# Optimization experiments

Hardware: AMD Instinct MI355X
Metric: run time of the kernel (lower is better)

## Reference

```python
import jax, jax.numpy as jnp
import numpy as np


def _init_t_xy(end_x, end_y):
    t = jnp.arange(end_x * end_y, dtype=jnp.float32)
    return t % end_x, jnp.floor(t / end_x)


def _cis_cos_sin(freqs, t_x, t_y):
    # freqs: [2, H, D/4]; returns cos/sin of angles [H, N, D/2]
    fx = jnp.einsum('n,hd->hnd', t_x, freqs[0])
    fy = jnp.einsum('n,hd->hnd', t_y, freqs[1])
    ang = jnp.concatenate([fx, fy], axis=-1)
    return jnp.cos(ang), jnp.sin(ang)


def _rotate(x, c, s):
    # x: [B,H,N,D]; c,s: [H,N,D/2]; complex multiply in real arithmetic
    B, H, N, D = x.shape
    xr = x.reshape(B, H, N, D // 2, 2)
    x0, x1 = xr[..., 0], xr[..., 1]
    o0 = x0 * c[None] - x1 * s[None]
    o1 = x0 * s[None] + x1 * c[None]
    return jnp.stack([o0, o1], axis=-1).reshape(B, H, N, D)


def setup_inputs() -> dict:
    key = jax.random.key(0)
    k1, k2, k3, k4 = jax.random.split(key, 4)
    B, H, N, D = 2, 12, 2048, 64
    return {
        'q': jax.random.normal(k1, (B, H, N, D), dtype=jnp.float32),
        'b': jax.random.normal(k2, (B, H, N, D), dtype=jnp.float32),
        'rope_freqs': jax.random.normal(k3, (2, H, D // 4), dtype=jnp.float32),
        'weight': jax.random.uniform(k4, (1, H, 1, 1), dtype=jnp.float32),
        'end_x_xq': 64, 'end_y_xq': 32, 'end_x_xb': 64, 'end_y_xb': 32,
    }


def reference(q, b, rope_freqs, weight, end_x_xq, end_y_xq, end_x_xb, end_y_xb):
    t_x_xb, t_y_xb = _init_t_xy(end_x_xb, end_y_xb)
    t_x_xq, t_y_xq = _init_t_xy(end_x_xq, end_y_xq)
    # resample key-grid coordinates onto query grid
    t_x_xb = jnp.floor((t_x_xb + 0.5) / end_x_xb * end_x_xq - 0.5)
    t_y_xb = jnp.floor((t_y_xb + 0.5) / end_y_xb * end_y_xq - 0.5)
    ck, sk = _cis_cos_sin(rope_freqs, t_x_xb, t_y_xb)
    cq, sq = _cis_cos_sin(rope_freqs, t_x_xq, t_y_xq)
    # O(Nq*Nb) distance-decay mask, per-head decay rate
    dist = jnp.sqrt((t_x_xb[None, :] - t_x_xq[:, None]) ** 2
                    + (t_y_xb[None, :] - t_y_xq[:, None]) ** 2)
    delta = jnp.exp(-dist[None, None] * jax.nn.leaky_relu(weight))
    xq = _rotate(q, cq, sq)
    xb = _rotate(b, ck, sk)
    return jnp.einsum('bhnd,bhmd->bhnm', xq, xb) * delta
```

## Files before the change

kernel.cpp:

```cpp
#include <hip/hip_runtime.h>
#include <hip/hip_bf16.h>

#define BQ   2
#define NH   12
#define SEQ  2048
#define DIM  64
#define EXQ  64

#define TENSOR_ELEMS ((size_t)BQ * NH * SEQ * DIM)
#define ROPE_BLOCKS  6144

typedef __attribute__((ext_vector_type(8))) short short8;
typedef __attribute__((ext_vector_type(4))) float f32x4;

static __device__ __forceinline__ unsigned int pk2bf(float lo, float hi) {
    union { float f; unsigned int u; } a, b; a.f = lo; b.f = hi;
    unsigned int rl = (a.u + 0x7fffu + ((a.u >> 16) & 1u)) >> 16;
    unsigned int rh = (b.u + 0x7fffu + ((b.u >> 16) & 1u)) >> 16;
    return (rh << 16) | (rl & 0xffffu);
}

__global__ __launch_bounds__(256)
void rope_kernel(const float* __restrict__ qin,
                 const float* __restrict__ bin,
                 const float* __restrict__ freqs,
                 unsigned int* __restrict__ ws_u32)
{
    int t  = blockIdx.x * 256 + threadIdx.x;
    int p4 = t & 15;
    int n  = (t >> 4) & (SEQ - 1);
    int rest = t >> 15;
    int h    = rest % NH;
    int tb   = rest / NH;
    int tensor = tb >> 1;
    int b      = tb & 1;

    float tx = (float)(n & (EXQ - 1));
    float ty = (float)(n >> 6);

    int pr0 = 2 * p4;
    float f0, f1;
    if (p4 < 8) {
        f0 = freqs[h * 16 + pr0] * tx;
        f1 = freqs[h * 16 + pr0 + 1] * tx;
    } else {
        f0 = freqs[NH * 16 + h * 16 + (pr0 - 16)] * ty;
        f1 = freqs[NH * 16 + h * 16 + (pr0 - 15)] * ty;
    }

    const float* src = tensor ? bin : qin;
    size_t off = ((size_t)(b * NH + h) * SEQ + n) * DIM + 4 * p4;
    float4 v = *reinterpret_cast<const float4*>(src + off);

    float s0 = sinf(f0), c0 = cosf(f0);
    float s1 = sinf(f1), c1 = cosf(f1);

    float o0 = v.x * c0 - v.y * s0;
    float o1 = v.x * s0 + v.y * c0;
    float o2 = v.z * c1 - v.w * s1;
    float o3 = v.z * s1 + v.w * c1;

    uint2 packed;
    packed.x = pk2bf(o0, o1);
    packed.y = pk2bf(o2, o3);
    size_t uidx = (size_t)tensor * (TENSOR_ELEMS / 2) + (off >> 1);
    *reinterpret_cast<uint2*>(ws_u32 + uidx) = packed;
}

__global__ __launch_bounds__(256, 3)
void gemm_delta_kernel(const unsigned short* __restrict__ ws,
                       const float* __restrict__ weight,
                       float* __restrict__ out)
{
    __shared__ float lds[64 * 128];
    __shared__ float ltab[4 * 3 * 128];

    const int bh   = blockIdx.z;
    const int h    = bh % NH;
    const int lane = threadIdx.x & 63;
    const int wave = threadIdx.x >> 6;
    const int wr   = wave >> 1, wc = wave & 1;
    const int brow0 = blockIdx.y * 128;
    const int bcol0 = blockIdx.x * 128;
    const int row0 = brow0 + wr * 64;
    const int col0 = bcol0 + wc * 64;

    const unsigned short* xq = ws;
    const unsigned short* xb = ws + TENSOR_ELEMS;

    const int r16 = lane & 15;
    const int kg  = lane >> 4;

    const size_t base = (size_t)bh * SEQ * DIM;

    const float w  = weight[h];
    const float lw = w > 0.f ? w : 0.01f * w;
    const float scale = -lw * 1.44269504088896f;
    const int dymid = (bcol0 >> 6) - (brow0 >> 6);
    for (int e = threadIdx.x; e < 4 * 3 * 128; e += 256) {
        int x    = e & 127;
        int rest = e >> 7;
        int s    = rest / 3;
        int dyr  = rest - 3 * s;
        float dx = (float)(x + s - 63);
        float dy = (float)(dymid + dyr - 1);
        ltab[e] = exp2f(scale * sqrtf(dx * dx + dy * dy));
    }
    __syncthreads();

    f32x4 acc[4][4];
#pragma unroll
    for (int i = 0; i < 4; ++i)
#pragma unroll
        for (int j = 0; j < 4; ++j)
            acc[i][j] = (f32x4){0.f, 0.f, 0.f, 0.f};

#pragma unroll
    for (int kk = 0; kk < 2; ++kk) {
        short8 afr[4], bfr[4];
        int k = kk * 32 + kg * 8;
#pragma unroll
        for (int i = 0; i < 4; ++i) {
            int arw = row0 + i * 16 + r16;
            int bcl = col0 + i * 16 + r16;
            afr[i] = *reinterpret_cast<const short8*>(xq + base + (size_t)arw * DIM + k);
            bfr[i] = *reinterpret_cast<const short8*>(xb + base + (size_t)bcl * DIM + k);
        }
#pragma unroll
        for (int i = 0; i < 4; ++i)
#pragma unroll
            for (int j = 0; j < 4; ++j)
                acc[i][j] = __builtin_amdgcn_mfma_f32_16x16x32_bf16(
                    bfr[j], afr[i], acc[i][j], 0, 0, 0);
    }

    const int dyrel = (wc - wr) + 1;

#pragma unroll
    for (int half = 0; half < 2; ++half) {
        if (half) __syncthreads();
#pragma unroll
        for (int ii = 0; ii < 2; ++ii) {
            const int i  = half * 2 + ii;
            const int qx = i * 16 + r16;
            const int lrow = wr * 32 + ii * 16 + r16;
#pragma unroll
            for (int j = 0; j < 4; ++j) {
                int dxi_s = 63 - qx + kg * 4 + j * 16;
                int s     = dxi_s & 3;
                int tbase = dxi_s - s;
                f32x4 t = *reinterpret_cast<const f32x4*>(
                    &ltab[(s * 3 + dyrel) * 128 + tbase]);
                int col16 = wc * 16 + j * 4 + kg;
                int slot  = col16 ^ (lrow & 7);
                *reinterpret_cast<f32x4*>(&lds[lrow * 128 + slot * 4]) =
                    acc[i][j] * t;
            }
        }
        __syncthreads();
        const int c32 = lane & 31;
#pragma unroll
        for (int tI = 0; tI < 8; ++tI) {
            int lr = wave * 16 + tI * 2 + (lane >> 5);
            int slot = c32 ^ (lr & 7);
            f32x4 v = *reinterpret_cast<const f32x4*>(&lds[lr * 128 + slot * 4]);
            int wr_ = lr >> 5;
            int i   = half * 2 + ((lr >> 4) & 1);
            int grow = brow0 + wr_ * 64 + i * 16 + (lr & 15);
            float* op = out + ((size_t)bh * SEQ + grow) * SEQ + bcol0 + c32 * 4;
            __builtin_nontemporal_store(v, reinterpret_cast<f32x4*>(op));
        }
    }
}

extern "C" void kernel_launch(void* const* d_in, const int* in_sizes, int n_in,
                              void* d_out, int out_size, void* d_ws, size_t ws_size,
                              hipStream_t stream) {
    const float* q  = (const float*)d_in[0];
    const float* b  = (const float*)d_in[1];
    const float* fr = (const float*)d_in[2];
    const float* wt = (const float*)d_in[3];
    float* out = (float*)d_out;

    const size_t need_tensors = 2 * TENSOR_ELEMS * sizeof(unsigned short);
    if (ws_size < need_tensors) return;

    unsigned short* ws16 = (unsigned short*)d_ws;

    rope_kernel<<<ROPE_BLOCKS, 256, 0, stream>>>(q, b, fr, (unsigned int*)d_ws);

    dim3 grid(SEQ / 128, SEQ / 128, BQ * NH);
    gemm_delta_kernel<<<grid, 256, 0, stream>>>(ws16, wt, out);
}
```

Measured before the change: 104.5 us.

## Make GEMM-delta kernel persistent with prefetched fragments and register-computed decay

Replaces the 3D grid with 512 persistent blocks that each process 12 consecutive output tiles. The next tile's A/B fragments are prefetched during the epilogue, and the A panel is reused when the row panel is unchanged. The LDS decay table is dropped: decay factors are computed in registers per tile (28 exp2/sqrt per lane), and the whole 128x128 tile is staged through a doubled LDS buffer in one pass. The kernel is output-write bound, so the gain depends on overlapping stores with compute. Occupancy drops to 2 blocks per CU and register pressure rises.

After: 100.1 us. 1.04x faster.

```diff
diff --git a/kernel.cpp b/kernel.cpp
--- a/kernel.cpp
+++ b/kernel.cpp
@@ -9,6 +9,8 @@
 
 #define TENSOR_ELEMS ((size_t)BQ * NH * SEQ * DIM)
 #define ROPE_BLOCKS  6144
+#define PERS_BLOCKS  512
+#define TILES_PER_BLOCK 12
 
 typedef __attribute__((ext_vector_type(8))) short short8;
 typedef __attribute__((ext_vector_type(4))) float f32x4;
@@ -18,6 +20,11 @@
     unsigned int rl = (a.u + 0x7fffu + ((a.u >> 16) & 1u)) >> 16;
     unsigned int rh = (b.u + 0x7fffu + ((b.u >> 16) & 1u)) >> 16;
     return (rh << 16) | (rl & 0xffffu);
+}
+
+static __device__ __forceinline__ void wg_barrier_lds() {
+    asm volatile("s_waitcnt lgkmcnt(0)" ::: "memory");
+    __builtin_amdgcn_s_barrier();
 }
 
 __global__ __launch_bounds__(256)
@@ -67,107 +74,124 @@
     *reinterpret_cast<uint2*>(ws_u32 + uidx) = packed;
 }
 
-__global__ __launch_bounds__(256, 3)
+__global__ __launch_bounds__(256, 2)
 void gemm_delta_kernel(const unsigned short* __restrict__ ws,
                        const float* __restrict__ weight,
                        float* __restrict__ out)
 {
-    __shared__ float lds[64 * 128];
-    __shared__ float ltab[4 * 3 * 128];
-
-    const int bh   = blockIdx.z;
-    const int h    = bh % NH;
+    __shared__ float lds[128 * 128];
+
     const int lane = threadIdx.x & 63;
     const int wave = threadIdx.x >> 6;
     const int wr   = wave >> 1, wc = wave & 1;
-    const int brow0 = blockIdx.y * 128;
-    const int bcol0 = blockIdx.x * 128;
-    const int row0 = brow0 + wr * 64;
-    const int col0 = bcol0 + wc * 64;
+    const int r16  = lane & 15;
+    const int kg   = lane >> 4;
+    const int c32  = lane & 31;
 
     const unsigned short* xq = ws;
     const unsigned short* xb = ws + TENSOR_ELEMS;
 
-    const int r16 = lane & 15;
-    const int kg  = lane >> 4;
-
-    const size_t base = (size_t)bh * SEQ * DIM;
-
-    const float w  = weight[h];
-    const float lw = w > 0.f ? w : 0.01f * w;
-    const float scale = -lw * 1.44269504088896f;
-    const int dymid = (bcol0 >> 6) - (brow0 >> 6);
-    for (int e = threadIdx.x; e < 4 * 3 * 128; e += 256) {
-        int x    = e & 127;
-        int rest = e >> 7;
-        int s    = rest / 3;
-        int dyr  = rest - 3 * s;
-        float dx = (float)(x + s - 63);
-        float dy = (float)(dymid + dyr - 1);
-        ltab[e] = exp2f(scale * sqrtf(dx * dx + dy * dy));
-    }
-    __syncthreads();
-
-    f32x4 acc[4][4];
-#pragma unroll
-    for (int i = 0; i < 4; ++i)
-#pragma unroll
-        for (int j = 0; j < 4; ++j)
-            acc[i][j] = (f32x4){0.f, 0.f, 0.f, 0.f};
-
-#pragma unroll
-    for (int kk = 0; kk < 2; ++kk) {
-        short8 afr[4], bfr[4];
-        int k = kk * 32 + kg * 8;
+    short8 afr[2][4], bfr[2][4];
+    int last_panel = -1;
+
+    auto load_frags = [&](int g) {
+        int bh = g >> 8, rem = g & 255;
+        int trow = rem >> 4, tcol = rem & 15;
+        const size_t base = (size_t)bh * SEQ * DIM;
+        int panel = (bh << 4) | trow;
+        if (panel != last_panel) {
+            last_panel = panel;
+            int row0 = trow * 128 + wr * 64;
+#pragma unroll
+            for (int kk = 0; kk < 2; ++kk)
+#pragma unroll
+                for (int i = 0; i < 4; ++i) {
+                    int arw = row0 + i * 16 + r16;
+                    afr[kk][i] = *reinterpret_cast<const short8*>(
+                        xq + base + (size_t)arw * DIM + kk * 32 + kg * 8);
+                }
+        }
+        int col0 = tcol * 128 + wc * 64;
+#pragma unroll
+        for (int kk = 0; kk < 2; ++kk)
+#pragma unroll
+            for (int i = 0; i < 4; ++i) {
+                int bcl = col0 + i * 16 + r16;
+                bfr[kk][i] = *reinterpret_cast<const short8*>(
+                    xb + base + (size_t)bcl * DIM + kk * 32 + kg * 8);
+            }
+    };
+
+    int g0 = blockIdx.x * TILES_PER_BLOCK;
+    load_frags(g0);
+
+    for (int t = 0; t < TILES_PER_BLOCK; ++t) {
+        const int g    = g0 + t;
+        const int bh   = g >> 8, rem = g & 255;
+        const int trow = rem >> 4, tcol = rem & 15;
+        const int h    = bh % NH;
+        const int brow0 = trow * 128, bcol0 = tcol * 128;
+
+        f32x4 acc[4][4];
+#pragma unroll
+        for (int i = 0; i < 4; ++i)
+#pragma unroll
+            for (int j = 0; j < 4; ++j)
+                acc[i][j] = (f32x4){0.f, 0.f, 0.f, 0.f};
+#pragma unroll
+        for (int kk = 0; kk < 2; ++kk)
+#pragma unroll
+            for (int i = 0; i < 4; ++i)
+#pragma unroll
+                for (int j = 0; j < 4; ++j)
+                    acc[i][j] = __builtin_amdgcn_mfma_f32_16x16x32_bf16(
+                        bfr[kk][j], afr[kk][i], acc[i][j], 0, 0, 0);
+
+        {
+            float w  = weight[h];
+            float lw = w > 0.f ? w : 0.01f * w;
+            float scale = -lw * 1.44269504088896f;
+            float fdy = (float)(2 * (tcol - trow) + (wc - wr));
+            float dy2 = fdy * fdy;
+            f32x4 T[7];
+#pragma unroll
+            for (int d = 0; d < 7; ++d) {
+                float dx0 = (float)((d - 3) * 16 + kg * 4 - r16);
+#pragma unroll
+                for (int w_ = 0; w_ < 4; ++w_) {
+                    float dx = dx0 + (float)w_;
+                    T[d][w_] = exp2f(scale * sqrtf(dx * dx + dy2));
+                }
+            }
+#pragma unroll
+            for (int i = 0; i < 4; ++i)
+#pragma unroll
+                for (int j = 0; j < 4; ++j)
+                    acc[i][j] *= T[j - i + 3];
+        }
+
+        if (t + 1 < TILES_PER_BLOCK) load_frags(g + 1);
+        __builtin_amdgcn_sched_barrier(0);
+
+        wg_barrier_lds();
 #pragma unroll
         for (int i = 0; i < 4; ++i) {
-            int arw = row0 + i * 16 + r16;
-            int bcl = col0 + i * 16 + r16;
-            afr[i] = *reinterpret_cast<const short8*>(xq + base + (size_t)arw * DIM + k);
-            bfr[i] = *reinterpret_cast<const short8*>(xb + base + (size_t)bcl * DIM + k);
-        }
-#pragma unroll
-        for (int i = 0; i < 4; ++i)
-#pragma unroll
-            for (int j = 0; j < 4; ++j)
-                acc[i][j] = __builtin_amdgcn_mfma_f32_16x16x32_bf16(
-                    bfr[j], afr[i], acc[i][j], 0, 0, 0);
-    }
-
-    const int dyrel = (wc - wr) + 1;
-
-#pragma unroll
-    for (int half = 0; half < 2; ++half) {
-        if (half) __syncthreads();
-#pragma unroll
-        for (int ii = 0; ii < 2; ++ii) {
-            const int i  = half * 2 + ii;
-            const int qx = i * 16 + r16;
-            const int lrow = wr * 32 + ii * 16 + r16;
+            int lrow = wr * 64 + i * 16 + r16;
 #pragma unroll
             for (int j = 0; j < 4; ++j) {
-                int dxi_s = 63 - qx + kg * 4 + j * 16;
-                int s     = dxi_s & 3;
-                int tbase = dxi_s - s;
-                f32x4 t = *reinterpret_cast<const f32x4*>(
-                    &ltab[(s * 3 + dyrel) * 128 + tbase]);
-                int col16 = wc * 16 + j * 4 + kg;
-                int slot  = col16 ^ (lrow & 7);
-                *reinterpret_cast<f32x4*>(&lds[lrow * 128 + slot * 4]) =
-                    acc[i][j] * t;
+                int slot = (wc * 16 + j * 4 + kg) ^ (lrow & 7);
+                *reinterpret_cast<f32x4*>(&lds[lrow * 128 + slot * 4]) = acc[i][j];
             }
         }
-        __syncthreads();
-        const int c32 = lane & 31;
-#pragma unroll
-        for (int tI = 0; tI < 8; ++tI) {
-            int lr = wave * 16 + tI * 2 + (lane >> 5);
+        wg_barrier_lds();
+
+        const size_t obase = (size_t)bh * SEQ * SEQ;
+#pragma unroll
+        for (int tI = 0; tI < 16; ++tI) {
+            int lr = wave * 32 + tI * 2 + (lane >> 5);
             int slot = c32 ^ (lr & 7);
             f32x4 v = *reinterpret_cast<const f32x4*>(&lds[lr * 128 + slot * 4]);
-            int wr_ = lr >> 5;
-            int i   = half * 2 + ((lr >> 4) & 1);
-            int grow = brow0 + wr_ * 64 + i * 16 + (lr & 15);
-            float* op = out + ((size_t)bh * SEQ + grow) * SEQ + bcol0 + c32 * 4;
+            float* op = out + obase + (size_t)(brow0 + lr) * SEQ + bcol0 + c32 * 4;
             __builtin_nontemporal_store(v, reinterpret_cast<f32x4*>(op));
         }
     }
@@ -182,13 +206,11 @@
     const float* wt = (const float*)d_in[3];
     float* out = (float*)d_out;
 
-    const size_t need_tensors = 2 * TENSOR_ELEMS * sizeof(unsigned short);
-    if (ws_size < need_tensors) return;
-
-    unsigned short* ws16 = (unsigned short*)d_ws;
+    const size_t need = 2 * TENSOR_ELEMS * sizeof(unsigned short);
+    if (ws_size < need) return;
 
     rope_kernel<<<ROPE_BLOCKS, 256, 0, stream>>>(q, b, fr, (unsigned int*)d_ws);
 
-    dim3 grid(SEQ / 128, SEQ / 128, BQ * NH);
-    gemm_delta_kernel<<<grid, 256, 0, stream>>>(ws16, wt, out);
-}
+    gemm_delta_kernel<<<PERS_BLOCKS, 256, 0, stream>>>(
+        (const unsigned short*)d_ws, wt, out);
+}
```
